# Kernel optimization log

Measured on AMD Instinct MI355X. Metric: run time of the kernel, lower is better.

Reference implementation:

```python
import jax, jax.numpy as jnp
import numpy as np
from jax import lax

B, S, H = 2, 512, 2048          # batch, seq, hidden_size
I = 768                          # moe_intermediate_size
E = 64                           # num_experts
K = 8                            # num_experts_per_tok (top_k)


def setup_inputs() -> dict:
    key = jax.random.key(0)
    k1, k2, k3, k4 = jax.random.split(key, 4)
    hidden_states = jax.random.normal(k1, (B, S, H), jnp.float32)
    gate_weight = jax.random.normal(k2, (E, H), jnp.float32) * 0.02
    gate_up_weights = jax.random.normal(k3, (E, H, 2 * I), jnp.float32) * 0.02
    down_weights = jax.random.normal(k4, (E, I, H), jnp.float32) * 0.02
    return {
        "hidden_states": hidden_states,
        "gate_weight": gate_weight,
        "gate_up_weights": gate_up_weights,
        "down_weights": down_weights,
    }


def reference(hidden_states, gate_weight, gate_up_weights, down_weights):
    orig_shape = hidden_states.shape
    x = hidden_states.reshape(-1, H)          # [T, H]
    T = x.shape[0]

    # Router: softmax in fp32, top-k, renormalize (norm_topk_prob=True)
    logits = x @ gate_weight.T                # [T, E]
    probs = jax.nn.softmax(logits.astype(jnp.float32), axis=-1)
    routing_weights, selected_experts = lax.top_k(probs, K)   # [T, K]
    wsum = routing_weights.sum(axis=-1, keepdims=True)
    wsum = jnp.where(wsum == 0, 1.0, wsum)
    routing_weights = (routing_weights / wsum).astype(x.dtype)

    # Dense combine matrix [T, E]: zero weight for unselected experts.
    combine = jnp.zeros((T, E), x.dtype).at[
        jnp.arange(T)[:, None], selected_experts
    ].add(routing_weights)

    # Scan over experts; each step is one batched GEMM over all tokens,
    # masked/weighted by the combine weights (same math as per-token loop).
    def body(acc, ws):
        wgu, wd, we = ws                      # [H,2I], [I,H], [T]
        gu = x @ wgu                          # [T, 2I]
        gate, up = jnp.split(gu, 2, axis=-1)  # [T, I] each
        act = jax.nn.silu(gate) * up          # SwiGLU
        out = act @ wd                        # [T, H]
        return acc + we[:, None] * out, None

    init = jnp.zeros_like(x)
    final, _ = lax.scan(body, init, (gate_up_weights, down_weights, combine.T))
    return final.reshape(orig_shape)
```

## Files before the change

kernel.cpp:

```cpp
#include <hip/hip_runtime.h>
#include <hip/hip_bf16.h>
#include <hip/hip_fp16.h>

typedef unsigned int uint32;
typedef unsigned short u16;

#define TOK 1024
#define HID 2048
#define NEXP 64
#define TOPK 8
#define IMED 768
#define IMED2 1536

typedef __attribute__((ext_vector_type(8))) _Float16 half8;
typedef __attribute__((ext_vector_type(4))) float f32x4;

static __device__ __forceinline__ uint32 pack2(float a, float b) {
  union { _Float16 h[2]; uint32 u; } p;
  p.h[0] = (_Float16)a; p.h[1] = (_Float16)b;
  return p.u;
}
static __device__ __forceinline__ u16 f2h(float a) {
  union { _Float16 h; u16 u; } p;
  p.h = (_Float16)a;
  return p.u;
}

__global__ __launch_bounds__(256) void router_kernel(
    const float* __restrict__ x, const float* __restrict__ gw,
    int* __restrict__ topk_id, float* __restrict__ topk_w,
    u16* __restrict__ xh) {
  int t0 = blockIdx.x << 2;
  __shared__ float part[4][NEXP][5];
  int tid = threadIdx.x;
  int e = tid & 63, p = tid >> 6;
  const float* gwp = gw + (size_t)e * HID + (p << 9);
  const float* xp = x + (size_t)t0 * HID + (p << 9);
  float acc[4] = {0.f, 0.f, 0.f, 0.f};
  for (int i = 0; i < 128; i++) {
    float4 w = ((const float4*)gwp)[i];
    #pragma unroll
    for (int t = 0; t < 4; t++) {
      float4 xv = *(const float4*)(xp + (size_t)t * HID + (i << 2));
      acc[t] += w.x * xv.x + w.y * xv.y + w.z * xv.z + w.w * xv.w;
    }
  }
  #pragma unroll
  for (int t = 0; t < 4; t++) part[p][e][t] = acc[t];
  for (int i = tid; i < 2048; i += 256) {
    int r = i >> 9;
    int c = i & 511;
    float4 v = *(const float4*)(x + (size_t)(t0 + r) * HID + (c << 2));
    uint2 hp;
    hp.x = pack2(v.x, v.y);
    hp.y = pack2(v.z, v.w);
    *(uint2*)(xh + (size_t)(t0 + r) * HID + (c << 2)) = hp;
  }
  __syncthreads();
  int wv = tid >> 6, l = tid & 63;
  int t = t0 + wv;
  float lg = part[0][l][wv] + part[1][l][wv] + part[2][l][wv] + part[3][l][wv];
  float m = lg;
  #pragma unroll
  for (int d = 1; d < 64; d <<= 1) m = fmaxf(m, __shfl_xor(m, d));
  float v = __expf(lg - m);
  float w8[TOPK]; int i8[TOPK]; float wsum = 0.f;
  #pragma unroll
  for (int k = 0; k < TOPK; k++) {
    float bv = v; int bi = l;
    #pragma unroll
    for (int d = 1; d < 64; d <<= 1) {
      float ov = __shfl_xor(bv, d);
      int oi = __shfl_xor(bi, d);
      if (ov > bv || (ov == bv && oi < bi)) { bv = ov; bi = oi; }
    }
    w8[k] = bv; i8[k] = bi; wsum += bv;
    if (l == bi) v = -1.f;
  }
  if (l == 0) {
    float rinv = 1.f / wsum;
    #pragma unroll
    for (int k = 0; k < TOPK; k++) {
      topk_id[t * TOPK + k] = i8[k];
      topk_w[t * TOPK + k] = w8[k] * rinv;
    }
  }
}

__global__ __launch_bounds__(256) void scan_scatter_kernel(
    const int* __restrict__ topk_id, const float* __restrict__ topk_w,
    int* __restrict__ off, int* __restrict__ row_tok, float* __restrict__ row_w) {
  __shared__ int scnt[NEXP];
  __shared__ int soff[NEXP + 1];
  __shared__ int scur[NEXP];
  int tid = threadIdx.x;
  if (tid < NEXP) scnt[tid] = 0;
  __syncthreads();
  for (int i = tid; i < TOK * TOPK; i += 256) atomicAdd(&scnt[topk_id[i]], 1);
  __syncthreads();
  if (tid == 0) {
    int a = 0;
    for (int e = 0; e < NEXP; e++) { soff[e] = a; a += scnt[e]; }
    soff[NEXP] = a;
  }
  __syncthreads();
  if (tid < NEXP) scur[tid] = soff[tid];
  __syncthreads();
  for (int i = tid; i < TOK * TOPK; i += 256) {
    int e = topk_id[i];
    int p = atomicAdd(&scur[e], 1);
    row_tok[p] = i >> 3;
    row_w[p] = topk_w[i];
  }
  if (tid < NEXP + 1) off[tid] = soff[tid];
}

__global__ __launch_bounds__(512, 2) void gateup_kernel(
    const u16* __restrict__ xh, const float* __restrict__ Wgu,
    const int* __restrict__ off, const int* __restrict__ row_tok,
    u16* __restrict__ act) {
  int bid = blockIdx.x;
  int xcd = bid & 7, s2 = bid >> 3;
  int e = xcd + ((s2 & 7) << 3);
  int slab = s2 >> 3;
  int r0 = off[e];
  int ne = off[e + 1] - r0;
  int c0 = slab * 96;

  __shared__ __align__(16) char AsB[256 * 80];
  __shared__ __align__(16) char BsB[192 * 80];

  int tid = threadIdx.x;
  int lane = tid & 63;
  int wid = tid >> 6;
  int wm = wid >> 1, wn = wid & 1;
  int fr = lane & 15, hi = lane >> 4;

  int arow = tid >> 1, aseg = tid & 1;
  int tok = row_tok[r0 + ((arow < ne) ? arow : 0)];
  const u16* xa = xh + (size_t)tok * HID + (aseg << 4);
  int axr = (arow >> 2) & 3;

  bool bact = tid < 384;
  int cg = tid % 24, h = (tid / 24) & 1, kq = tid / 48;
  int bcol = cg << 2;
  int gc = h ? (IMED + c0 + bcol) : (c0 + bcol);
  const float* wb = Wgu + (size_t)e * ((size_t)HID * IMED2) + (size_t)(kq << 2) * IMED2 + gc;
  int brbase = 96 * h + bcol;

  f32x4 accg[4][3], accu[4][3];
  #pragma unroll
  for (int a = 0; a < 4; a++)
    #pragma unroll
    for (int b = 0; b < 3; b++) { accg[a][b] = (f32x4)0.f; accu[a][b] = (f32x4)0.f; }

  uint4 qa0, qa1;
  float4 w0, w1, w2, w3;
  auto LOADT = [&]() {
    const uint4* p = (const uint4*)xa;
    qa0 = p[0]; qa1 = p[1];
    xa += 32;
    if (bact) {
      w0 = *(const float4*)(wb);
      w1 = *(const float4*)(wb + IMED2);
      w2 = *(const float4*)(wb + 2 * IMED2);
      w3 = *(const float4*)(wb + 3 * IMED2);
    }
    wb += (size_t)32 * IMED2;
  };
  auto STORET = [&]() {
    char* A_ = AsB + arow * 80;
    int g0 = aseg << 1;
    *(uint4*)(A_ + (((g0 + 0) ^ axr) << 4)) = qa0;
    *(uint4*)(A_ + (((g0 + 1) ^ axr) << 4)) = qa1;
    if (bact) {
      float c0v[4] = {w0.x, w0.y, w0.z, w0.w};
      float c1v[4] = {w1.x, w1.y, w1.z, w1.w};
      float c2v[4] = {w2.x, w2.y, w2.z, w2.w};
      float c3v[4] = {w3.x, w3.y, w3.z, w3.w};
      int kg = kq >> 1, kb = (kq & 1) << 3;
      #pragma unroll
      for (int cc = 0; cc < 4; cc++) {
        int br = brbase + cc;
        uint2 pv;
        pv.x = pack2(c0v[cc], c1v[cc]);
        pv.y = pack2(c2v[cc], c3v[cc]);
        *(uint2*)(BsB + br * 80 + (((kg ^ (br >> 2)) & 3) << 4) + kb) = pv;
      }
    }
  };

  const int NK = HID / 32;
  LOADT();
  STORET();
  LOADT();
  __syncthreads();

  for (int t = 0; t < NK; ++t) {
    half8 af[4];
    #pragma unroll
    for (int mi = 0; mi < 4; mi++) {
      int r = (wm << 6) + (mi << 4) + fr;
      af[mi] = *(half8*)(AsB + r * 80 + (((hi ^ (r >> 2)) & 3) << 4));
    }
    #pragma unroll
    for (int ni = 0; ni < 3; ni++) {
      int ng = (wn * 48) + (ni << 4) + fr;
      int nu = ng + 96;
      half8 bg = *(half8*)(BsB + ng * 80 + (((hi ^ (ng >> 2)) & 3) << 4));
      half8 bu = *(half8*)(BsB + nu * 80 + (((hi ^ (nu >> 2)) & 3) << 4));
      #pragma unroll
      for (int mi = 0; mi < 4; mi++) {
        accg[mi][ni] = __builtin_amdgcn_mfma_f32_16x16x32_f16(af[mi], bg, accg[mi][ni], 0, 0, 0);
        accu[mi][ni] = __builtin_amdgcn_mfma_f32_16x16x32_f16(af[mi], bu, accu[mi][ni], 0, 0, 0);
      }
    }
    __syncthreads();
    if (t + 1 < NK) {
      STORET();
      if (t + 2 < NK) LOADT();
      __syncthreads();
    }
  }

  #pragma unroll
  for (int mi = 0; mi < 4; mi++) {
    #pragma unroll
    for (int ni = 0; ni < 3; ni++) {
      int col = c0 + wn * 48 + (ni << 4) + fr;
      #pragma unroll
      for (int r = 0; r < 4; r++) {
        int rr = (wm << 6) + (mi << 4) + (hi << 2) + r;
        if (rr < ne) {
          float g = accg[mi][ni][r];
          float u = accu[mi][ni][r];
          float s = g / (1.f + __expf(-g)) * u;
          act[(size_t)(r0 + rr) * IMED + col] = f2h(s);
        }
      }
    }
  }
}

__global__ __launch_bounds__(512, 2) void down_kernel(
    const u16* __restrict__ act, const float* __restrict__ Wd,
    const int* __restrict__ off, const int* __restrict__ row_tok,
    const float* __restrict__ row_w, float* __restrict__ out) {
  int bid = blockIdx.x;
  int xcd = bid & 7, s2 = bid >> 3;
  int e = xcd + ((s2 & 7) << 3);
  int slab = s2 >> 3;
  int r0 = off[e];
  int ne = off[e + 1] - r0;
  int n0 = slab << 8;

  __shared__ __align__(16) char AsB[256 * 80];
  __shared__ __align__(16) char BsB[256 * 80];

  int tid = threadIdx.x;
  int lane = tid & 63;
  int wid = tid >> 6;
  int wm = wid >> 1, wn = wid & 1;
  int fr = lane & 15, hi = lane >> 4;

  int arow = tid >> 1, aseg = tid & 1;
  const u16* ap = act + (size_t)(r0 + ((arow < ne) ? arow : 0)) * IMED + (aseg << 4);
  int axr = (arow >> 2) & 3;

  int cq = tid & 63, kq = tid >> 6;
  int bcol = cq << 2;
  const float* wb = Wd + (size_t)e * ((size_t)IMED * HID) + (size_t)(kq << 2) * HID + n0 + bcol;

  f32x4 acc[4][8];
  #pragma unroll
  for (int a = 0; a < 4; a++)
    #pragma unroll
    for (int b = 0; b < 8; b++) acc[a][b] = (f32x4)0.f;

  uint4 qa0, qa1;
  float4 w0, w1, w2, w3;
  auto LOADT = [&]() {
    const uint4* p = (const uint4*)ap;
    qa0 = p[0]; qa1 = p[1];
    ap += 32;
    w0 = *(const float4*)(wb);
    w1 = *(const float4*)(wb + HID);
    w2 = *(const float4*)(wb + 2 * HID);
    w3 = *(const float4*)(wb + 3 * HID);
    wb += (size_t)32 * HID;
  };
  auto STORET = [&]() {
    char* A_ = AsB + arow * 80;
    int g0 = aseg << 1;
    *(uint4*)(A_ + (((g0 + 0) ^ axr) << 4)) = qa0;
    *(uint4*)(A_ + (((g0 + 1) ^ axr) << 4)) = qa1;
    float c0v[4] = {w0.x, w0.y, w0.z, w0.w};
    float c1v[4] = {w1.x, w1.y, w1.z, w1.w};
    float c2v[4] = {w2.x, w2.y, w2.z, w2.w};
    float c3v[4] = {w3.x, w3.y, w3.z, w3.w};
    int kg = kq >> 1, kb = (kq & 1) << 3;
    #pragma unroll
    for (int cc = 0; cc < 4; cc++) {
      int br = bcol + cc;
      uint2 pv;
      pv.x = pack2(c0v[cc], c1v[cc]);
      pv.y = pack2(c2v[cc], c3v[cc]);
      *(uint2*)(BsB + br * 80 + (((kg ^ (br >> 2)) & 3) << 4) + kb) = pv;
    }
  };

  const int NK = IMED / 32;
  LOADT();
  STORET();
  LOADT();
  __syncthreads();

  for (int t = 0; t < NK; ++t) {
    half8 af[4];
    #pragma unroll
    for (int mi = 0; mi < 4; mi++) {
      int r = (wm << 6) + (mi << 4) + fr;
      af[mi] = *(half8*)(AsB + r * 80 + (((hi ^ (r >> 2)) & 3) << 4));
    }
    #pragma unroll
    for (int ni = 0; ni < 8; ni++) {
      int n = (wn << 7) + (ni << 4) + fr;
      half8 bf_ = *(half8*)(BsB + n * 80 + (((hi ^ (n >> 2)) & 3) << 4));
      #pragma unroll
      for (int mi = 0; mi < 4; mi++)
        acc[mi][ni] = __builtin_amdgcn_mfma_f32_16x16x32_f16(af[mi], bf_, acc[mi][ni], 0, 0, 0);
    }
    __syncthreads();
    if (t + 1 < NK) {
      STORET();
      if (t + 2 < NK) LOADT();
      __syncthreads();
    }
  }

  #pragma unroll
  for (int mi = 0; mi < 4; mi++) {
    #pragma unroll
    for (int r = 0; r < 4; r++) {
      int rr = (wm << 6) + (mi << 4) + (hi << 2) + r;
      if (rr < ne) {
        float w = row_w[r0 + rr];
        int t = row_tok[r0 + rr];
        #pragma unroll
        for (int ni = 0; ni < 8; ni++) {
          int col = n0 + (wn << 7) + (ni << 4) + fr;
          unsafeAtomicAdd(&out[(size_t)t * HID + col], acc[mi][ni][r] * w);
        }
      }
    }
  }
}

extern "C" void kernel_launch(void* const* d_in, const int* in_sizes, int n_in,
                              void* d_out, int out_size, void* d_ws, size_t ws_size,
                              hipStream_t stream) {
  const float* x = (const float*)d_in[0];
  const float* gw = (const float*)d_in[1];
  const float* wgu = (const float*)d_in[2];
  const float* wd = (const float*)d_in[3];
  float* out = (float*)d_out;
  char* ws = (char*)d_ws;

  int* off = (int*)(ws + 0);
  int* topk_id = (int*)(ws + 1024);
  float* topk_w = (float*)(ws + 1024 + 32768);
  int* row_tok = (int*)(ws + 1024 + 65536);
  float* row_w = (float*)(ws + 1024 + 98304);
  u16* act = (u16*)(ws + 135168);
  u16* xh = (u16*)(ws + 135168 + (size_t)TOK * TOPK * IMED * 2);

  router_kernel<<<TOK / 4, 256, 0, stream>>>(x, gw, topk_id, topk_w, xh);
  scan_scatter_kernel<<<1, 256, 0, stream>>>(topk_id, topk_w, off, row_tok, row_w);
  hipMemsetAsync(out, 0, (size_t)TOK * HID * sizeof(float), stream);
  gateup_kernel<<<512, 512, 0, stream>>>(xh, wgu, off, row_tok, act);
  down_kernel<<<512, 512, 0, stream>>>(act, wd, off, row_tok, row_w, out);
}
```

Before: 392.9 us.

## Parallelize expert scatter per expert and double-buffer register prefetch in GEMMs

The router now counts tokens per expert with global atomics. The single-block scan/scatter is replaced by one block per expert that computes its prefix offset with a wave scan and gathers only its own rows. In both GEMM kernels, register-staged global loads are now double-buffered, so two K-tiles are in flight ahead of the LDS store. This aims to hide more global memory latency, at the cost of more registers and an extra memset launch. Row order within an expert is now nondeterministic, but the results are unaffected apart from atomic-add ordering.

After: 425.1 us. +8.2%, slower.

```diff
diff --git a/kernel.cpp b/kernel.cpp
--- a/kernel.cpp
+++ b/kernel.cpp
@@ -29,7 +29,7 @@
 __global__ __launch_bounds__(256) void router_kernel(
     const float* __restrict__ x, const float* __restrict__ gw,
     int* __restrict__ topk_id, float* __restrict__ topk_w,
-    u16* __restrict__ xh) {
+    u16* __restrict__ xh, int* __restrict__ cnt) {
   int t0 = blockIdx.x << 2;
   __shared__ float part[4][NEXP][5];
   int tid = threadIdx.x;
@@ -83,48 +83,110 @@
     for (int k = 0; k < TOPK; k++) {
       topk_id[t * TOPK + k] = i8[k];
       topk_w[t * TOPK + k] = w8[k] * rinv;
-    }
-  }
-}
-
-__global__ __launch_bounds__(256) void scan_scatter_kernel(
+      atomicAdd(&cnt[i8[k]], 1);
+    }
+  }
+}
+
+__global__ __launch_bounds__(256) void scatter_kernel(
     const int* __restrict__ topk_id, const float* __restrict__ topk_w,
-    int* __restrict__ off, int* __restrict__ row_tok, float* __restrict__ row_w) {
-  __shared__ int scnt[NEXP];
-  __shared__ int soff[NEXP + 1];
-  __shared__ int scur[NEXP];
+    const int* __restrict__ cnt, int* __restrict__ off,
+    int* __restrict__ row_tok, float* __restrict__ row_w) {
+  int e = blockIdx.x;
+  __shared__ int sbase;
+  __shared__ int scur;
   int tid = threadIdx.x;
-  if (tid < NEXP) scnt[tid] = 0;
+  if (tid < 64) {
+    int c = cnt[tid];
+    int xv = c;
+    #pragma unroll
+    for (int d = 1; d < 64; d <<= 1) {
+      int y = __shfl_up(xv, d);
+      if (tid >= d) xv += y;
+    }
+    if (tid == e) { sbase = xv - c; off[e] = xv - c; }
+    if (tid == 0) scur = 0;
+  }
   __syncthreads();
-  for (int i = tid; i < TOK * TOPK; i += 256) atomicAdd(&scnt[topk_id[i]], 1);
-  __syncthreads();
-  if (tid == 0) {
-    int a = 0;
-    for (int e = 0; e < NEXP; e++) { soff[e] = a; a += scnt[e]; }
-    soff[NEXP] = a;
-  }
-  __syncthreads();
-  if (tid < NEXP) scur[tid] = soff[tid];
-  __syncthreads();
+  int base = sbase;
   for (int i = tid; i < TOK * TOPK; i += 256) {
-    int e = topk_id[i];
-    int p = atomicAdd(&scur[e], 1);
-    row_tok[p] = i >> 3;
-    row_w[p] = topk_w[i];
-  }
-  if (tid < NEXP + 1) off[tid] = soff[tid];
-}
+    if (topk_id[i] == e) {
+      int p = atomicAdd(&scur, 1);
+      row_tok[base + p] = i >> 3;
+      row_w[base + p] = topk_w[i];
+    }
+  }
+}
+
+#define GU_LOAD(S)                                                        \
+  {                                                                       \
+    const uint4* p_ = (const uint4*)xa;                                   \
+    qa0_##S = p_[0]; qa1_##S = p_[1];                                     \
+    xa += 32;                                                             \
+    if (bact) {                                                           \
+      w0_##S = *(const float4*)(wb);                                      \
+      w1_##S = *(const float4*)(wb + IMED2);                              \
+      w2_##S = *(const float4*)(wb + 2 * IMED2);                          \
+      w3_##S = *(const float4*)(wb + 3 * IMED2);                          \
+    }                                                                     \
+    wb += (size_t)32 * IMED2;                                             \
+  }
+
+#define GU_STORE(S)                                                       \
+  {                                                                       \
+    char* A_ = AsB + arow * 80;                                           \
+    int g0 = aseg << 1;                                                   \
+    *(uint4*)(A_ + (((g0 + 0) ^ axr) << 4)) = qa0_##S;                    \
+    *(uint4*)(A_ + (((g0 + 1) ^ axr) << 4)) = qa1_##S;                    \
+    if (bact) {                                                           \
+      float c0v[4] = {w0_##S.x, w0_##S.y, w0_##S.z, w0_##S.w};            \
+      float c1v[4] = {w1_##S.x, w1_##S.y, w1_##S.z, w1_##S.w};            \
+      float c2v[4] = {w2_##S.x, w2_##S.y, w2_##S.z, w2_##S.w};            \
+      float c3v[4] = {w3_##S.x, w3_##S.y, w3_##S.z, w3_##S.w};            \
+      int kg = kq >> 1, kb = (kq & 1) << 3;                               \
+      _Pragma("unroll")                                                   \
+      for (int cc = 0; cc < 4; cc++) {                                    \
+        int br = brbase + cc;                                             \
+        uint2 pv;                                                         \
+        pv.x = pack2(c0v[cc], c1v[cc]);                                   \
+        pv.y = pack2(c2v[cc], c3v[cc]);                                   \
+        *(uint2*)(BsB + br * 80 + (((kg ^ (br >> 2)) & 3) << 4) + kb) = pv; \
+      }                                                                   \
+    }                                                                     \
+  }
+
+#define GU_COMPUTE()                                                      \
+  {                                                                       \
+    half8 af[4];                                                          \
+    _Pragma("unroll")                                                     \
+    for (int mi = 0; mi < 4; mi++) {                                      \
+      int r = (wm << 6) + (mi << 4) + fr;                                 \
+      af[mi] = *(half8*)(AsB + r * 80 + (((hi ^ (r >> 2)) & 3) << 4));    \
+    }                                                                     \
+    _Pragma("unroll")                                                     \
+    for (int ni = 0; ni < 3; ni++) {                                      \
+      int ng = (wn * 48) + (ni << 4) + fr;                                \
+      int nu = ng + 96;                                                   \
+      half8 bg = *(half8*)(BsB + ng * 80 + (((hi ^ (ng >> 2)) & 3) << 4)); \
+      half8 bu = *(half8*)(BsB + nu * 80 + (((hi ^ (nu >> 2)) & 3) << 4)); \
+      _Pragma("unroll")                                                   \
+      for (int mi = 0; mi < 4; mi++) {                                    \
+        accg[mi][ni] = __builtin_amdgcn_mfma_f32_16x16x32_f16(af[mi], bg, accg[mi][ni], 0, 0, 0); \
+        accu[mi][ni] = __builtin_amdgcn_mfma_f32_16x16x32_f16(af[mi], bu, accu[mi][ni], 0, 0, 0); \
+      }                                                                   \
+    }                                                                     \
+  }
 
 __global__ __launch_bounds__(512, 2) void gateup_kernel(
     const u16* __restrict__ xh, const float* __restrict__ Wgu,
-    const int* __restrict__ off, const int* __restrict__ row_tok,
-    u16* __restrict__ act) {
+    const int* __restrict__ off, const int* __restrict__ cnt,
+    const int* __restrict__ row_tok, u16* __restrict__ act) {
   int bid = blockIdx.x;
   int xcd = bid & 7, s2 = bid >> 3;
   int e = xcd + ((s2 & 7) << 3);
   int slab = s2 >> 3;
   int r0 = off[e];
-  int ne = off[e + 1] - r0;
+  int ne = cnt[e];
   int c0 = slab * 96;
 
   __shared__ __align__(16) char AsB[256 * 80];
@@ -154,71 +216,27 @@
     #pragma unroll
     for (int b = 0; b < 3; b++) { accg[a][b] = (f32x4)0.f; accu[a][b] = (f32x4)0.f; }
 
-  uint4 qa0, qa1;
-  float4 w0, w1, w2, w3;
-  auto LOADT = [&]() {
-    const uint4* p = (const uint4*)xa;
-    qa0 = p[0]; qa1 = p[1];
-    xa += 32;
-    if (bact) {
-      w0 = *(const float4*)(wb);
-      w1 = *(const float4*)(wb + IMED2);
-      w2 = *(const float4*)(wb + 2 * IMED2);
-      w3 = *(const float4*)(wb + 3 * IMED2);
-    }
-    wb += (size_t)32 * IMED2;
-  };
-  auto STORET = [&]() {
-    char* A_ = AsB + arow * 80;
-    int g0 = aseg << 1;
-    *(uint4*)(A_ + (((g0 + 0) ^ axr) << 4)) = qa0;
-    *(uint4*)(A_ + (((g0 + 1) ^ axr) << 4)) = qa1;
-    if (bact) {
-      float c0v[4] = {w0.x, w0.y, w0.z, w0.w};
-      float c1v[4] = {w1.x, w1.y, w1.z, w1.w};
-      float c2v[4] = {w2.x, w2.y, w2.z, w2.w};
-      float c3v[4] = {w3.x, w3.y, w3.z, w3.w};
-      int kg = kq >> 1, kb = (kq & 1) << 3;
-      #pragma unroll
-      for (int cc = 0; cc < 4; cc++) {
-        int br = brbase + cc;
-        uint2 pv;
-        pv.x = pack2(c0v[cc], c1v[cc]);
-        pv.y = pack2(c2v[cc], c3v[cc]);
-        *(uint2*)(BsB + br * 80 + (((kg ^ (br >> 2)) & 3) << 4) + kb) = pv;
-      }
-    }
-  };
+  uint4 qa0_0, qa1_0, qa0_1, qa1_1;
+  float4 w0_0, w1_0, w2_0, w3_0, w0_1, w1_1, w2_1, w3_1;
 
   const int NK = HID / 32;
-  LOADT();
-  STORET();
-  LOADT();
+  GU_LOAD(0);
+  GU_LOAD(1);
+  GU_STORE(0);
+  GU_LOAD(0);
   __syncthreads();
 
-  for (int t = 0; t < NK; ++t) {
-    half8 af[4];
-    #pragma unroll
-    for (int mi = 0; mi < 4; mi++) {
-      int r = (wm << 6) + (mi << 4) + fr;
-      af[mi] = *(half8*)(AsB + r * 80 + (((hi ^ (r >> 2)) & 3) << 4));
-    }
-    #pragma unroll
-    for (int ni = 0; ni < 3; ni++) {
-      int ng = (wn * 48) + (ni << 4) + fr;
-      int nu = ng + 96;
-      half8 bg = *(half8*)(BsB + ng * 80 + (((hi ^ (ng >> 2)) & 3) << 4));
-      half8 bu = *(half8*)(BsB + nu * 80 + (((hi ^ (nu >> 2)) & 3) << 4));
-      #pragma unroll
-      for (int mi = 0; mi < 4; mi++) {
-        accg[mi][ni] = __builtin_amdgcn_mfma_f32_16x16x32_f16(af[mi], bg, accg[mi][ni], 0, 0, 0);
-        accu[mi][ni] = __builtin_amdgcn_mfma_f32_16x16x32_f16(af[mi], bu, accu[mi][ni], 0, 0, 0);
-      }
-    }
-    __syncthreads();
-    if (t + 1 < NK) {
-      STORET();
-      if (t + 2 < NK) LOADT();
+  for (int t = 0; t < NK; t += 2) {
+    GU_COMPUTE();
+    __syncthreads();
+    GU_STORE(1);
+    if (t + 3 < NK) GU_LOAD(1);
+    __syncthreads();
+    GU_COMPUTE();
+    __syncthreads();
+    if (t + 2 < NK) {
+      GU_STORE(0);
+      if (t + 4 < NK) GU_LOAD(0);
       __syncthreads();
     }
   }
@@ -242,16 +260,68 @@
   }
 }
 
+#define DN_LOAD(S)                                                        \
+  {                                                                       \
+    const uint4* p_ = (const uint4*)ap;                                   \
+    qa0_##S = p_[0]; qa1_##S = p_[1];                                     \
+    ap += 32;                                                             \
+    w0_##S = *(const float4*)(wb);                                        \
+    w1_##S = *(const float4*)(wb + HID);                                  \
+    w2_##S = *(const float4*)(wb + 2 * HID);                              \
+    w3_##S = *(const float4*)(wb + 3 * HID);                              \
+    wb += (size_t)32 * HID;                                               \
+  }
+
+#define DN_STORE(S)                                                       \
+  {                                                                       \
+    char* A_ = AsB + arow * 80;                                           \
+    int g0 = aseg << 1;                                                   \
+    *(uint4*)(A_ + (((g0 + 0) ^ axr) << 4)) = qa0_##S;                    \
+    *(uint4*)(A_ + (((g0 + 1) ^ axr) << 4)) = qa1_##S;                    \
+    float c0v[4] = {w0_##S.x, w0_##S.y, w0_##S.z, w0_##S.w};              \
+    float c1v[4] = {w1_##S.x, w1_##S.y, w1_##S.z, w1_##S.w};              \
+    float c2v[4] = {w2_##S.x, w2_##S.y, w2_##S.z, w2_##S.w};              \
+    float c3v[4] = {w3_##S.x, w3_##S.y, w3_##S.z, w3_##S.w};              \
+    int kg = kq >> 1, kb = (kq & 1) << 3;                                 \
+    _Pragma("unroll")                                                     \
+    for (int cc = 0; cc < 4; cc++) {                                      \
+      int br = bcol + cc;                                                 \
+      uint2 pv;                                                           \
+      pv.x = pack2(c0v[cc], c1v[cc]);                                     \
+      pv.y = pack2(c2v[cc], c3v[cc]);                                     \
+      *(uint2*)(BsB + br * 80 + (((kg ^ (br >> 2)) & 3) << 4) + kb) = pv; \
+    }                                                                     \
+  }
+
+#define DN_COMPUTE()                                                      \
+  {                                                                       \
+    half8 af[4];                                                          \
+    _Pragma("unroll")                                                     \
+    for (int mi = 0; mi < 4; mi++) {                                      \
+      int r = (wm << 6) + (mi << 4) + fr;                                 \
+      af[mi] = *(half8*)(AsB + r * 80 + (((hi ^ (r >> 2)) & 3) << 4));    \
+    }                                                                     \
+    _Pragma("unroll")                                                     \
+    for (int ni = 0; ni < 8; ni++) {                                      \
+      int n = (wn << 7) + (ni << 4) + fr;                                 \
+      half8 bf_ = *(half8*)(BsB + n * 80 + (((hi ^ (n >> 2)) & 3) << 4)); \
+      _Pragma("unroll")                                                   \
+      for (int mi = 0; mi < 4; mi++)                                      \
+        acc[mi][ni] = __builtin_amdgcn_mfma_f32_16x16x32_f16(af[mi], bf_, acc[mi][ni], 0, 0, 0); \
+    }                                                                     \
+  }
+
 __global__ __launch_bounds__(512, 2) void down_kernel(
     const u16* __restrict__ act, const float* __restrict__ Wd,
-    const int* __restrict__ off, const int* __restrict__ row_tok,
-    const float* __restrict__ row_w, float* __restrict__ out) {
+    const int* __restrict__ off, const int* __restrict__ cnt,
+    const int* __restrict__ row_tok, const float* __restrict__ row_w,
+    float* __restrict__ out) {
   int bid = blockIdx.x;
   int xcd = bid & 7, s2 = bid >> 3;
   int e = xcd + ((s2 & 7) << 3);
   int slab = s2 >> 3;
   int r0 = off[e];
-  int ne = off[e + 1] - r0;
+  int ne = cnt[e];
   int n0 = slab << 8;
 
   __shared__ __align__(16) char AsB[256 * 80];
@@ -277,63 +347,27 @@
     #pragma unroll
     for (int b = 0; b < 8; b++) acc[a][b] = (f32x4)0.f;
 
-  uint4 qa0, qa1;
-  float4 w0, w1, w2, w3;
-  auto LOADT = [&]() {
-    const uint4* p = (const uint4*)ap;
-    qa0 = p[0]; qa1 = p[1];
-    ap += 32;
-    w0 = *(const float4*)(wb);
-    w1 = *(const float4*)(wb + HID);
-    w2 = *(const float4*)(wb + 2 * HID);
-    w3 = *(const float4*)(wb + 3 * HID);
-    wb += (size_t)32 * HID;
-  };
-  auto STORET = [&]() {
-    char* A_ = AsB + arow * 80;
-    int g0 = aseg << 1;
-    *(uint4*)(A_ + (((g0 + 0) ^ axr) << 4)) = qa0;
-    *(uint4*)(A_ + (((g0 + 1) ^ axr) << 4)) = qa1;
-    float c0v[4] = {w0.x, w0.y, w0.z, w0.w};
-    float c1v[4] = {w1.x, w1.y, w1.z, w1.w};
-    float c2v[4] = {w2.x, w2.y, w2.z, w2.w};
-    float c3v[4] = {w3.x, w3.y, w3.z, w3.w};
-    int kg = kq >> 1, kb = (kq & 1) << 3;
-    #pragma unroll
-    for (int cc = 0; cc < 4; cc++) {
-      int br = bcol + cc;
-      uint2 pv;
-      pv.x = pack2(c0v[cc], c1v[cc]);
-      pv.y = pack2(c2v[cc], c3v[cc]);
-      *(uint2*)(BsB + br * 80 + (((kg ^ (br >> 2)) & 3) << 4) + kb) = pv;
-    }
-  };
+  uint4 qa0_0, qa1_0, qa0_1, qa1_1;
+  float4 w0_0, w1_0, w2_0, w3_0, w0_1, w1_1, w2_1, w3_1;
 
   const int NK = IMED / 32;
-  LOADT();
-  STORET();
-  LOADT();
+  DN_LOAD(0);
+  DN_LOAD(1);
+  DN_STORE(0);
+  DN_LOAD(0);
   __syncthreads();
 
-  for (int t = 0; t < NK; ++t) {
-    half8 af[4];
-    #pragma unroll
-    for (int mi = 0; mi < 4; mi++) {
-      int r = (wm << 6) + (mi << 4) + fr;
-      af[mi] = *(half8*)(AsB + r * 80 + (((hi ^ (r >> 2)) & 3) << 4));
-    }
-    #pragma unroll
-    for (int ni = 0; ni < 8; ni++) {
-      int n = (wn << 7) + (ni << 4) + fr;
-      half8 bf_ = *(half8*)(BsB + n * 80 + (((hi ^ (n >> 2)) & 3) << 4));
-      #pragma unroll
-      for (int mi = 0; mi < 4; mi++)
-        acc[mi][ni] = __builtin_amdgcn_mfma_f32_16x16x32_f16(af[mi], bf_, acc[mi][ni], 0, 0, 0);
-    }
-    __syncthreads();
-    if (t + 1 < NK) {
-      STORET();
-      if (t + 2 < NK) LOADT();
+  for (int t = 0; t < NK; t += 2) {
+    DN_COMPUTE();
+    __syncthreads();
+    DN_STORE(1);
+    if (t + 3 < NK) DN_LOAD(1);
+    __syncthreads();
+    DN_COMPUTE();
+    __syncthreads();
+    if (t + 2 < NK) {
+      DN_STORE(0);
+      if (t + 4 < NK) DN_LOAD(0);
       __syncthreads();
     }
   }
@@ -366,7 +400,8 @@
   float* out = (float*)d_out;
   char* ws = (char*)d_ws;
 
-  int* off = (int*)(ws + 0);
+  int* cnt = (int*)(ws + 0);
+  int* off = (int*)(ws + 512);
   int* topk_id = (int*)(ws + 1024);
   float* topk_w = (float*)(ws + 1024 + 32768);
   int* row_tok = (int*)(ws + 1024 + 65536);
@@ -374,9 +409,10 @@
   u16* act = (u16*)(ws + 135168);
   u16* xh = (u16*)(ws + 135168 + (size_t)TOK * TOPK * IMED * 2);
 
-  router_kernel<<<TOK / 4, 256, 0, stream>>>(x, gw, topk_id, topk_w, xh);
-  scan_scatter_kernel<<<1, 256, 0, stream>>>(topk_id, topk_w, off, row_tok, row_w);
+  hipMemsetAsync(cnt, 0, 256, stream);
+  router_kernel<<<TOK / 4, 256, 0, stream>>>(x, gw, topk_id, topk_w, xh, cnt);
+  scatter_kernel<<<NEXP, 256, 0, stream>>>(topk_id, topk_w, cnt, off, row_tok, row_w);
   hipMemsetAsync(out, 0, (size_t)TOK * HID * sizeof(float), stream);
-  gateup_kernel<<<512, 512, 0, stream>>>(xh, wgu, off, row_tok, act);
-  down_kernel<<<512, 512, 0, stream>>>(act, wd, off, row_tok, row_w, out);
-}
+  gateup_kernel<<<512, 512, 0, stream>>>(xh, wgu, off, cnt, row_tok, act);
+  down_kernel<<<512, 512, 0, stream>>>(act, wd, off, cnt, row_tok, row_w, out);
+}
```

## Replace atomic output accumulation with fp16 scratch and gather combine kernel

Applied to the files above, without the earlier changes.

Per-expert counts now come from atomics in the router, and the single-block scan/scatter becomes a 64-block per-expert scatter that also records each token-slot's row index. The down projection writes weighted fp16 rows to scratch instead of atomically adding into the fp32 output. A new combine kernel gathers each token's 8 rows and sums them, which removes the output memset and the atomic contention. The cost is an extra kernel launch, scratch traffic, and fp16 rounding of the partial outputs.

New measurement: 398.4 us. No clear change (+1.4%).

```diff
diff --git a/kernel.cpp b/kernel.cpp
--- a/kernel.cpp
+++ b/kernel.cpp
@@ -29,7 +29,7 @@
 __global__ __launch_bounds__(256) void router_kernel(
     const float* __restrict__ x, const float* __restrict__ gw,
     int* __restrict__ topk_id, float* __restrict__ topk_w,
-    u16* __restrict__ xh) {
+    u16* __restrict__ xh, int* __restrict__ cnt) {
   int t0 = blockIdx.x << 2;
   __shared__ float part[4][NEXP][5];
   int tid = threadIdx.x;
@@ -83,48 +83,53 @@
     for (int k = 0; k < TOPK; k++) {
       topk_id[t * TOPK + k] = i8[k];
       topk_w[t * TOPK + k] = w8[k] * rinv;
-    }
-  }
-}
-
-__global__ __launch_bounds__(256) void scan_scatter_kernel(
+      atomicAdd(&cnt[i8[k]], 1);
+    }
+  }
+}
+
+__global__ __launch_bounds__(256) void scatter_kernel(
     const int* __restrict__ topk_id, const float* __restrict__ topk_w,
-    int* __restrict__ off, int* __restrict__ row_tok, float* __restrict__ row_w) {
-  __shared__ int scnt[NEXP];
-  __shared__ int soff[NEXP + 1];
-  __shared__ int scur[NEXP];
+    const int* __restrict__ cnt, int* __restrict__ off,
+    int* __restrict__ row_tok, float* __restrict__ row_w,
+    int* __restrict__ inv) {
+  int e = blockIdx.x;
+  __shared__ int sbase;
+  __shared__ int scur;
   int tid = threadIdx.x;
-  if (tid < NEXP) scnt[tid] = 0;
+  if (tid < 64) {
+    int c = cnt[tid];
+    int xv = c;
+    #pragma unroll
+    for (int d = 1; d < 64; d <<= 1) {
+      int y = __shfl_up(xv, d);
+      if (tid >= d) xv += y;
+    }
+    if (tid == e) { sbase = xv - c; off[e] = xv - c; }
+    if (tid == 0) scur = 0;
+  }
   __syncthreads();
-  for (int i = tid; i < TOK * TOPK; i += 256) atomicAdd(&scnt[topk_id[i]], 1);
-  __syncthreads();
-  if (tid == 0) {
-    int a = 0;
-    for (int e = 0; e < NEXP; e++) { soff[e] = a; a += scnt[e]; }
-    soff[NEXP] = a;
-  }
-  __syncthreads();
-  if (tid < NEXP) scur[tid] = soff[tid];
-  __syncthreads();
+  int base = sbase;
   for (int i = tid; i < TOK * TOPK; i += 256) {
-    int e = topk_id[i];
-    int p = atomicAdd(&scur[e], 1);
-    row_tok[p] = i >> 3;
-    row_w[p] = topk_w[i];
-  }
-  if (tid < NEXP + 1) off[tid] = soff[tid];
+    if (topk_id[i] == e) {
+      int p = atomicAdd(&scur, 1);
+      row_tok[base + p] = i >> 3;
+      row_w[base + p] = topk_w[i];
+      inv[i] = base + p;
+    }
+  }
 }
 
 __global__ __launch_bounds__(512, 2) void gateup_kernel(
     const u16* __restrict__ xh, const float* __restrict__ Wgu,
-    const int* __restrict__ off, const int* __restrict__ row_tok,
-    u16* __restrict__ act) {
+    const int* __restrict__ off, const int* __restrict__ cnt,
+    const int* __restrict__ row_tok, u16* __restrict__ act) {
   int bid = blockIdx.x;
   int xcd = bid & 7, s2 = bid >> 3;
   int e = xcd + ((s2 & 7) << 3);
   int slab = s2 >> 3;
   int r0 = off[e];
-  int ne = off[e + 1] - r0;
+  int ne = cnt[e];
   int c0 = slab * 96;
 
   __shared__ __align__(16) char AsB[256 * 80];
@@ -244,14 +249,14 @@
 
 __global__ __launch_bounds__(512, 2) void down_kernel(
     const u16* __restrict__ act, const float* __restrict__ Wd,
-    const int* __restrict__ off, const int* __restrict__ row_tok,
-    const float* __restrict__ row_w, float* __restrict__ out) {
+    const int* __restrict__ off, const int* __restrict__ cnt,
+    const float* __restrict__ row_w, u16* __restrict__ dscr) {
   int bid = blockIdx.x;
   int xcd = bid & 7, s2 = bid >> 3;
   int e = xcd + ((s2 & 7) << 3);
   int slab = s2 >> 3;
   int r0 = off[e];
-  int ne = off[e + 1] - r0;
+  int ne = cnt[e];
   int n0 = slab << 8;
 
   __shared__ __align__(16) char AsB[256 * 80];
@@ -345,15 +350,36 @@
       int rr = (wm << 6) + (mi << 4) + (hi << 2) + r;
       if (rr < ne) {
         float w = row_w[r0 + rr];
-        int t = row_tok[r0 + rr];
         #pragma unroll
         for (int ni = 0; ni < 8; ni++) {
           int col = n0 + (wn << 7) + (ni << 4) + fr;
-          unsafeAtomicAdd(&out[(size_t)t * HID + col], acc[mi][ni][r] * w);
+          dscr[(size_t)(r0 + rr) * HID + col] = f2h(acc[mi][ni][r] * w);
         }
       }
     }
   }
+}
+
+__global__ __launch_bounds__(256) void combine_kernel(
+    const u16* __restrict__ dscr, const int* __restrict__ inv,
+    float* __restrict__ out) {
+  int t = blockIdx.x;
+  int c0 = threadIdx.x << 3;
+  int rows[TOPK];
+  #pragma unroll
+  for (int k = 0; k < TOPK; k++) rows[k] = inv[t * TOPK + k];
+  float s[8] = {0.f, 0.f, 0.f, 0.f, 0.f, 0.f, 0.f, 0.f};
+  #pragma unroll
+  for (int k = 0; k < TOPK; k++) {
+    union { uint4 q; _Float16 h[8]; } u;
+    u.q = *(const uint4*)(dscr + (size_t)rows[k] * HID + c0);
+    #pragma unroll
+    for (int j = 0; j < 8; j++) s[j] += (float)u.h[j];
+  }
+  float4 o0 = {s[0], s[1], s[2], s[3]};
+  float4 o1 = {s[4], s[5], s[6], s[7]};
+  *(float4*)(out + (size_t)t * HID + c0) = o0;
+  *(float4*)(out + (size_t)t * HID + c0 + 4) = o1;
 }
 
 extern "C" void kernel_launch(void* const* d_in, const int* in_sizes, int n_in,
@@ -366,17 +392,21 @@
   float* out = (float*)d_out;
   char* ws = (char*)d_ws;
 
-  int* off = (int*)(ws + 0);
+  int* cnt = (int*)(ws + 0);
+  int* off = (int*)(ws + 512);
   int* topk_id = (int*)(ws + 1024);
   float* topk_w = (float*)(ws + 1024 + 32768);
   int* row_tok = (int*)(ws + 1024 + 65536);
   float* row_w = (float*)(ws + 1024 + 98304);
   u16* act = (u16*)(ws + 135168);
-  u16* xh = (u16*)(ws + 135168 + (size_t)TOK * TOPK * IMED * 2);
-
-  router_kernel<<<TOK / 4, 256, 0, stream>>>(x, gw, topk_id, topk_w, xh);
-  scan_scatter_kernel<<<1, 256, 0, stream>>>(topk_id, topk_w, off, row_tok, row_w);
-  hipMemsetAsync(out, 0, (size_t)TOK * HID * sizeof(float), stream);
-  gateup_kernel<<<512, 512, 0, stream>>>(xh, wgu, off, row_tok, act);
-  down_kernel<<<512, 512, 0, stream>>>(act, wd, off, row_tok, row_w, out);
-}
+  u16* xh = (u16*)(ws + 135168 + 12582912);
+  int* inv = (int*)(ws + 135168 + 12582912 + 4194304);
+  u16* dscr = (u16*)(ws + 135168 + 12582912 + 4194304 + 32768);
+
+  hipMemsetAsync(cnt, 0, 256, stream);
+  router_kernel<<<TOK / 4, 256, 0, stream>>>(x, gw, topk_id, topk_w, xh, cnt);
+  scatter_kernel<<<NEXP, 256, 0, stream>>>(topk_id, topk_w, cnt, off, row_tok, row_w, inv);
+  gateup_kernel<<<512, 512, 0, stream>>>(xh, wgu, off, cnt, row_tok, act);
+  down_kernel<<<512, 512, 0, stream>>>(act, wd, off, cnt, row_w, dscr);
+  combine_kernel<<<TOK, 256, 0, stream>>>(dscr, inv, out);
+}
```
